# Performance work log

Measured on AMD Instinct MI355X. Metric: run time of the kernel, lower is better.

Reference implementation:

```python
import math
import jax, jax.numpy as jnp
import numpy as np

INPUT_DIM = 1024
OUTPUT_DIM = 1024
DEGREE = 8
EPS = 1.0


def setup_inputs() -> dict:
    key = jax.random.key(0)
    k1, k2 = jax.random.split(key)
    x = jax.random.normal(k1, (8192, INPUT_DIM), dtype=jnp.float32)
    std = 1.0 / (INPUT_DIM * (DEGREE + 1))
    hermite_coeffs = std * jax.random.normal(k2, (INPUT_DIM, OUTPUT_DIM, DEGREE + 1), dtype=jnp.float32)
    return {"x": x, "hermite_coeffs": hermite_coeffs}


def _hermite_basis(x):
    # x: [B, I] squashed input; returns [B, I, DEGREE+1] Hermite-function basis.
    pi_q = math.pi ** (-0.25)
    gauss = jnp.exp(-0.5 * x * x)
    h0 = pi_q * gauss
    hs = [h0]
    if DEGREE > 0:
        hs.append(math.sqrt(2.0) * pi_q * x * gauss)
    for i in range(2, DEGREE + 1):
        hs.append(math.sqrt(2.0 / i) * x * hs[i - 1] - math.sqrt((i - 1) / i) * hs[i - 2])
    return jnp.stack(hs, axis=-1)


def reference(x, hermite_coeffs):
    x = x.reshape(-1, INPUT_DIM)
    x = jnp.tanh(x) * (math.sqrt(2 * DEGREE + 1) + EPS)
    hermite = _hermite_basis(x)  # [B, I, D+1]
    y = jnp.einsum('bid,iod->bo', hermite, hermite_coeffs)
    return y.reshape(-1, OUTPUT_DIM)
```

## Files before the change

### kernel.cpp

```cpp
#include <hip/hip_runtime.h>

#define MDIM 8192
#define IDIM 1024
#define ODIM 1024
#define D1   9
#define KDIM (IDIM * D1)

typedef _Float16 half8   __attribute__((ext_vector_type(8)));
typedef _Float16 half2v  __attribute__((ext_vector_type(2)));
typedef float    float4v __attribute__((ext_vector_type(4)));

#define BSCALE 256.0f
#define INV_BSCALE (1.0f / 256.0f)
#define USCALE 5.123105625617661f
#define H0C 0.7511255444649425f
#define H1C 1.0622519497598084f

__device__ __forceinline__ void hermite9(float xv, float h[D1]) {
    float ax = fabsf(xv);
    float t  = __expf(-2.0f * ax);
    float th = (1.0f - t) / (1.0f + t);
    th = copysignf(th, xv);
    float u = th * USCALE;
    float g = __expf(-0.5f * u * u);
    h[0] = H0C * g;
    h[1] = H1C * u * g;
    const float c1[D1] = {0.f, 0.f, 1.0f, 0.8164965809277260f, 0.7071067811865476f,
                          0.6324555320336759f, 0.5773502691896258f, 0.5345224838248488f, 0.5f};
    const float c2[D1] = {0.f, 0.f, 0.7071067811865476f, 0.8164965809277260f, 0.8660254037844386f,
                          0.8944271909999159f, 0.9128709291752769f, 0.9258200997725514f, 0.9354143466934853f};
#pragma unroll
    for (int d = 2; d < D1; ++d) h[d] = c1[d] * u * h[d - 1] - c2[d] * h[d - 2];
}

__global__ __launch_bounds__(256) void prep_b(const float* __restrict__ C,
                                              _Float16* __restrict__ Bt) {
    __shared__ float lds[288 * 33];
    const int t  = threadIdx.x;
    const int ti = blockIdx.x & 31;
    const int to = blockIdx.x >> 5;
    const float* base = C + (size_t)ti * 32 * 9216 + (size_t)to * 32 * 9;
#pragma unroll
    for (int j = 0; j < 36; ++j) {
        int f   = t + 256 * j;
        int row = f / 288;
        int col = f - row * 288;
        lds[col * 33 + row] = base[(size_t)row * 9216 + col];
    }
    __syncthreads();
    _Float16* bb = Bt + (size_t)to * 32 * KDIM + ti * 32;
#pragma unroll
    for (int j = 0; j < 36; ++j) {
        int e   = t + 256 * j;
        int i   = e & 31;
        int odp = e >> 5;
        int ol  = odp / 9;
        int d   = odp - ol * 9;
        bb[(size_t)ol * KDIM + d * IDIM + i] = (_Float16)(lds[odp * 33 + i] * BSCALE);
    }
}

__global__ __launch_bounds__(256, 2) void gemm_fused(
    const float* __restrict__ x,
    const _Float16* __restrict__ Bt,
    float* __restrict__ out)
{
    const int tid = threadIdx.x;
    const int w = tid >> 6;
    const int l = tid & 63;
    const int bn = blockIdx.x;
    const int bm = blockIdx.y;

    __shared__ _Float16 As[128 * 64];
    __shared__ _Float16 Bs[128 * 64];

    const int lrow8 = l >> 3;
    const int kgrp  = (l & 7) ^ lrow8;
    const _Float16* Bg = Bt + ((size_t)(bn * 128 + w * 8 + lrow8) * KDIM + kgrp * 8);

    const int q   = l >> 4;
    const int m16 = l & 15;
    const int s3  = m16 & 7;
    const int wm  = w >> 1, wn = w & 1;

    const int r  = tid >> 1;
    const int ih = tid & 1;
    const int r7 = r & 7;
    _Float16* arow = As + r * 64;

    float4v acc[4][4] = {};

    constexpr float c1a[D1] = {0.f, 0.f, 1.0f, 0.8164965809277260f, 0.7071067811865476f,
                               0.6324555320336759f, 0.5773502691896258f, 0.5345224838248488f, 0.5f};
    constexpr float c2a[D1] = {0.f, 0.f, 0.7071067811865476f, 0.8164965809277260f, 0.8660254037844386f,
                               0.8944271909999159f, 0.9128709291752769f, 0.9258200997725514f, 0.9354143466934853f};

    for (int ib = 0; ib < 16; ++ib) {
        const int kbase = ib * 64;

#pragma unroll
        for (int rr = 0; rr < 4; ++rr)
            __builtin_amdgcn_global_load_lds(
                (const __attribute__((address_space(1))) void*)(Bg + (size_t)(rr * 32) * KDIM + kbase),
                (__attribute__((address_space(3))) void*)((char*)Bs + (rr * 4 + w) * 1024),
                16, 0, 0);

        const float4* xp = (const float4*)(x + (((size_t)(bm * 128 + r)) << 10) + kbase + ih * 32);
        float u[32];
#pragma unroll
        for (int j = 0; j < 8; ++j) {
            float4 v = xp[j];
            u[4*j+0] = v.x; u[4*j+1] = v.y; u[4*j+2] = v.z; u[4*j+3] = v.w;
        }
#pragma unroll
        for (int j = 0; j < 32; ++j) {
            float xv = u[j];
            float t2 = __expf(-2.0f * fabsf(xv));
            float th = (1.0f - t2) / (1.0f + t2);
            u[j] = copysignf(th, xv) * USCALE;
        }
        half2v u2[16], hA[16], hB[16];
#pragma unroll
        for (int p = 0; p < 16; ++p) {
            float u0 = u[2*p], u1 = u[2*p+1];
            float g0 = __expf(-0.5f * u0 * u0);
            float g1 = __expf(-0.5f * u1 * u1);
            u2[p] = half2v{(_Float16)u0, (_Float16)u1};
            hA[p] = half2v{(_Float16)(H0C * g0), (_Float16)(H0C * g1)};
            hB[p] = half2v{(_Float16)(H1C * u0 * g0), (_Float16)(H1C * u1 * g1)};
        }

#pragma unroll
        for (int d = 0; d < D1; ++d) {
            if (d >= 1) {
#pragma unroll
                for (int rr = 0; rr < 4; ++rr)
                    __builtin_amdgcn_global_load_lds(
                        (const __attribute__((address_space(1))) void*)(Bg + (size_t)(rr * 32) * KDIM + d * IDIM + kbase),
                        (__attribute__((address_space(3))) void*)((char*)Bs + (rr * 4 + w) * 1024),
                        16, 0, 0);
            }
            half2v ht[16];
            if (d == 0) {
#pragma unroll
                for (int p = 0; p < 16; ++p) ht[p] = hA[p];
            } else if (d == 1) {
#pragma unroll
                for (int p = 0; p < 16; ++p) ht[p] = hB[p];
            } else {
                const half2v c1v = half2v{(_Float16)c1a[d], (_Float16)c1a[d]};
                const half2v c2v = half2v{(_Float16)c2a[d], (_Float16)c2a[d]};
#pragma unroll
                for (int p = 0; p < 16; ++p) {
                    half2v t = u2[p] * hB[p];
                    ht[p] = c1v * t - c2v * hA[p];
                    hA[p] = hB[p];
                    hB[p] = ht[p];
                }
            }
#pragma unroll
            for (int c = 0; c < 4; ++c) {
                int slot = (ih * 4 + c) ^ r7;
                half8 vv;
#pragma unroll
                for (int pp = 0; pp < 4; ++pp) {
                    vv[2*pp+0] = ht[4*c+pp][0];
                    vv[2*pp+1] = ht[4*c+pp][1];
                }
                *(half8*)(arow + slot * 8) = vv;
            }
            __syncthreads();

#pragma unroll
            for (int ko = 0; ko < 2; ++ko) {
                const int slot = (q + 4 * ko) ^ s3;
                half8 af[4], bf[4];
#pragma unroll
                for (int i = 0; i < 4; ++i) {
                    af[i] = *(const half8*)&As[(wm * 64 + i * 16 + m16) * 64 + slot * 8];
                    bf[i] = *(const half8*)&Bs[(wn * 64 + i * 16 + m16) * 64 + slot * 8];
                }
#pragma unroll
                for (int i = 0; i < 4; ++i)
#pragma unroll
                    for (int j = 0; j < 4; ++j)
                        acc[i][j] = __builtin_amdgcn_mfma_f32_16x16x32_f16(af[i], bf[j], acc[i][j], 0, 0, 0);
            }
            __syncthreads();
        }
    }

#pragma unroll
    for (int i = 0; i < 4; ++i) {
        int row = bm * 128 + wm * 64 + i * 16 + q * 4;
#pragma unroll
        for (int j = 0; j < 4; ++j) {
            int col = bn * 128 + wn * 64 + j * 16 + m16;
            float* op = out + (size_t)row * ODIM + col;
#pragma unroll
            for (int r2 = 0; r2 < 4; ++r2)
                op[(size_t)r2 * ODIM] = acc[i][j][r2] * INV_BSCALE;
        }
    }
}

__global__ void naive_kernel(const float* __restrict__ x, const float* __restrict__ C,
                             float* __restrict__ out) {
    __shared__ float hb[IDIM * D1];
    int b = blockIdx.x;
    int tid = threadIdx.x;
    for (int i = tid; i < IDIM; i += 256) {
        float h[D1];
        hermite9(x[(size_t)b * IDIM + i], h);
#pragma unroll
        for (int d = 0; d < D1; ++d) hb[i * D1 + d] = h[d];
    }
    __syncthreads();
    for (int o = tid; o < ODIM; o += 256) {
        float acc = 0.f;
        for (int i = 0; i < IDIM; ++i) {
            const float* cp = C + ((size_t)i * ODIM + o) * D1;
            const float* hp = hb + i * D1;
#pragma unroll
            for (int d = 0; d < D1; ++d) acc += hp[d] * cp[d];
        }
        out[(size_t)b * ODIM + o] = acc;
    }
}

extern "C" void kernel_launch(void* const* d_in, const int* in_sizes, int n_in,
                              void* d_out, int out_size, void* d_ws, size_t ws_size,
                              hipStream_t stream) {
    const float* x      = (const float*)d_in[0];
    const float* coeffs = (const float*)d_in[1];
    float* out = (float*)d_out;

    const size_t bt_bytes = (size_t)ODIM * KDIM * sizeof(_Float16);

    if (ws_size >= bt_bytes) {
        _Float16* Bt = (_Float16*)d_ws;
        hipLaunchKernelGGL(prep_b, dim3(1024), dim3(256), 0, stream, coeffs, Bt);
        hipLaunchKernelGGL(gemm_fused, dim3(8, 64), dim3(256), 0, stream, x, Bt, out);
    } else {
        hipLaunchKernelGGL(naive_kernel, dim3(MDIM), dim3(256), 0, stream, x, coeffs, out);
    }
}
```

Baseline: 313.9 us.

## Precompute tanh/gauss basis in separate kernel and double-buffer LDS tiles

Adds a prep_u kernel that computes the squashed input and the Gaussian term once per element in fp16. Each of the 8 column blocks then reads these instead of recomputing tanh and exp from the fp32 input. The GEMM kernel double-buffers the A and B LDS tiles, prefetching the next B tile and generating the next Hermite degree while the current tile runs through MFMA, which halves the barriers per step. In exchange it adds a kernel launch, extra workspace and global traffic for U and H0, doubles LDS use (which may limit occupancy), and rounds h1 to fp16 sooner.

```diff
diff --git a/kernel.cpp b/kernel.cpp
--- a/kernel.cpp
+++ b/kernel.cpp
@@ -14,7 +14,7 @@
 #define INV_BSCALE (1.0f / 256.0f)
 #define USCALE 5.123105625617661f
 #define H0C 0.7511255444649425f
-#define H1C 1.0622519497598084f
+#define SQRT2 1.4142135623730951f
 
 __device__ __forceinline__ void hermite9(float xv, float h[D1]) {
     float ax = fabsf(xv);
@@ -24,7 +24,7 @@
     float u = th * USCALE;
     float g = __expf(-0.5f * u * u);
     h[0] = H0C * g;
-    h[1] = H1C * u * g;
+    h[1] = SQRT2 * H0C * u * g;
     const float c1[D1] = {0.f, 0.f, 1.0f, 0.8164965809277260f, 0.7071067811865476f,
                           0.6324555320336759f, 0.5773502691896258f, 0.5345224838248488f, 0.5f};
     const float c2[D1] = {0.f, 0.f, 0.7071067811865476f, 0.8164965809277260f, 0.8660254037844386f,
@@ -60,8 +60,31 @@
     }
 }
 
-__global__ __launch_bounds__(256, 2) void gemm_fused(
-    const float* __restrict__ x,
+__global__ __launch_bounds__(256) void prep_u(const float* __restrict__ x,
+                                              _Float16* __restrict__ U,
+                                              _Float16* __restrict__ H0) {
+    size_t t = (size_t)blockIdx.x * 256 + threadIdx.x;
+    const float4* xp = (const float4*)(x + t * 8);
+    float4 a0 = xp[0], a1 = xp[1];
+    float xv[8] = {a0.x, a0.y, a0.z, a0.w, a1.x, a1.y, a1.z, a1.w};
+    half8 uu, hh;
+#pragma unroll
+    for (int e = 0; e < 8; ++e) {
+        float v  = xv[e];
+        float t2 = __expf(-2.0f * fabsf(v));
+        float th = (1.0f - t2) / (1.0f + t2);
+        float u  = copysignf(th, v) * USCALE;
+        float g  = __expf(-0.5f * u * u);
+        uu[e] = (_Float16)u;
+        hh[e] = (_Float16)(H0C * g);
+    }
+    *(half8*)(U  + t * 8) = uu;
+    *(half8*)(H0 + t * 8) = hh;
+}
+
+__global__ __launch_bounds__(256, 2) void gemm_fused2(
+    const _Float16* __restrict__ U,
+    const _Float16* __restrict__ H0,
     const _Float16* __restrict__ Bt,
     float* __restrict__ out)
 {
@@ -71,8 +94,8 @@
     const int bn = blockIdx.x;
     const int bm = blockIdx.y;
 
-    __shared__ _Float16 As[128 * 64];
-    __shared__ _Float16 Bs[128 * 64];
+    __shared__ _Float16 As[2][128 * 64];
+    __shared__ _Float16 Bs[2][128 * 64];
 
     const int lrow8 = l >> 3;
     const int kgrp  = (l & 7) ^ lrow8;
@@ -86,90 +109,102 @@
     const int r  = tid >> 1;
     const int ih = tid & 1;
     const int r7 = r & 7;
-    _Float16* arow = As + r * 64;
-
-    float4v acc[4][4] = {};
+    const size_t urow = (((size_t)(bm * 128 + r)) << 10) + ih * 32;
 
     constexpr float c1a[D1] = {0.f, 0.f, 1.0f, 0.8164965809277260f, 0.7071067811865476f,
                                0.6324555320336759f, 0.5773502691896258f, 0.5345224838248488f, 0.5f};
     constexpr float c2a[D1] = {0.f, 0.f, 0.7071067811865476f, 0.8164965809277260f, 0.8660254037844386f,
                                0.8944271909999159f, 0.9128709291752769f, 0.9258200997725514f, 0.9354143466934853f};
 
+    half2v u2[16], hA[16], hB[16];
+    const half2v sq2 = half2v{(_Float16)SQRT2, (_Float16)SQRT2};
+
+    auto loadUH = [&](int kb) {
+        const half8* up = (const half8*)(U  + urow + kb);
+        const half8* hp = (const half8*)(H0 + urow + kb);
+        half8 ub[4], hb[4];
+#pragma unroll
+        for (int a = 0; a < 4; ++a) { ub[a] = up[a]; hb[a] = hp[a]; }
+#pragma unroll
+        for (int a = 0; a < 4; ++a)
+#pragma unroll
+            for (int b = 0; b < 4; ++b) {
+                u2[4*a+b] = half2v{ub[a][2*b], ub[a][2*b+1]};
+                hA[4*a+b] = half2v{hb[a][2*b], hb[a][2*b+1]};
+            }
+#pragma unroll
+        for (int p = 0; p < 16; ++p) hB[p] = sq2 * u2[p] * hA[p];
+    };
+
+    _Float16* arow0 = &As[0][r * 64];
+    _Float16* arow1 = &As[1][r * 64];
+    auto writeA = [&](int buf, const half2v ht[16]) {
+        _Float16* arow = buf ? arow1 : arow0;
+#pragma unroll
+        for (int c = 0; c < 4; ++c) {
+            int slot = (ih * 4 + c) ^ r7;
+            half8 vv;
+#pragma unroll
+            for (int pp = 0; pp < 4; ++pp) {
+                vv[2*pp+0] = ht[4*c+pp][0];
+                vv[2*pp+1] = ht[4*c+pp][1];
+            }
+            *(half8*)(arow + slot * 8) = vv;
+        }
+    };
+
+    float4v acc[4][4] = {};
+
+#pragma unroll
+    for (int rr = 0; rr < 4; ++rr)
+        __builtin_amdgcn_global_load_lds(
+            (const __attribute__((address_space(1))) void*)(Bg + (size_t)(rr * 32) * KDIM),
+            (__attribute__((address_space(3))) void*)((char*)&Bs[0][0] + (rr * 4 + w) * 1024),
+            16, 0, 0);
+    loadUH(0);
+    writeA(0, hA);
+    __syncthreads();
+
     for (int ib = 0; ib < 16; ++ib) {
         const int kbase = ib * 64;
-
-#pragma unroll
-        for (int rr = 0; rr < 4; ++rr)
-            __builtin_amdgcn_global_load_lds(
-                (const __attribute__((address_space(1))) void*)(Bg + (size_t)(rr * 32) * KDIM + kbase),
-                (__attribute__((address_space(3))) void*)((char*)Bs + (rr * 4 + w) * 1024),
-                16, 0, 0);
-
-        const float4* xp = (const float4*)(x + (((size_t)(bm * 128 + r)) << 10) + kbase + ih * 32);
-        float u[32];
-#pragma unroll
-        for (int j = 0; j < 8; ++j) {
-            float4 v = xp[j];
-            u[4*j+0] = v.x; u[4*j+1] = v.y; u[4*j+2] = v.z; u[4*j+3] = v.w;
-        }
-#pragma unroll
-        for (int j = 0; j < 32; ++j) {
-            float xv = u[j];
-            float t2 = __expf(-2.0f * fabsf(xv));
-            float th = (1.0f - t2) / (1.0f + t2);
-            u[j] = copysignf(th, xv) * USCALE;
-        }
-        half2v u2[16], hA[16], hB[16];
-#pragma unroll
-        for (int p = 0; p < 16; ++p) {
-            float u0 = u[2*p], u1 = u[2*p+1];
-            float g0 = __expf(-0.5f * u0 * u0);
-            float g1 = __expf(-0.5f * u1 * u1);
-            u2[p] = half2v{(_Float16)u0, (_Float16)u1};
-            hA[p] = half2v{(_Float16)(H0C * g0), (_Float16)(H0C * g1)};
-            hB[p] = half2v{(_Float16)(H1C * u0 * g0), (_Float16)(H1C * u1 * g1)};
-        }
-
 #pragma unroll
         for (int d = 0; d < D1; ++d) {
-            if (d >= 1) {
+            const int cur = (ib + d) & 1;
+            const int nxt = cur ^ 1;
+            const bool has_next = (d < 8) || (ib < 15);
+
+            if (has_next) {
+                const int nkoff = (d == 8) ? (kbase + 64)
+                                           : ((d + 1) * IDIM + kbase);
 #pragma unroll
                 for (int rr = 0; rr < 4; ++rr)
                     __builtin_amdgcn_global_load_lds(
-                        (const __attribute__((address_space(1))) void*)(Bg + (size_t)(rr * 32) * KDIM + d * IDIM + kbase),
-                        (__attribute__((address_space(3))) void*)((char*)Bs + (rr * 4 + w) * 1024),
+                        (const __attribute__((address_space(1))) void*)(Bg + (size_t)(rr * 32) * KDIM + nkoff),
+                        (__attribute__((address_space(3))) void*)((char*)&Bs[nxt][0] + (rr * 4 + w) * 1024),
                         16, 0, 0);
             }
+
             half2v ht[16];
-            if (d == 0) {
-#pragma unroll
-                for (int p = 0; p < 16; ++p) ht[p] = hA[p];
-            } else if (d == 1) {
-#pragma unroll
-                for (int p = 0; p < 16; ++p) ht[p] = hB[p];
-            } else {
-                const half2v c1v = half2v{(_Float16)c1a[d], (_Float16)c1a[d]};
-                const half2v c2v = half2v{(_Float16)c2a[d], (_Float16)c2a[d]};
-#pragma unroll
-                for (int p = 0; p < 16; ++p) {
-                    half2v t = u2[p] * hB[p];
-                    ht[p] = c1v * t - c2v * hA[p];
-                    hA[p] = hB[p];
-                    hB[p] = ht[p];
+            if (has_next) {
+                if (d == 8) {
+                    loadUH(kbase + 64);
+#pragma unroll
+                    for (int p = 0; p < 16; ++p) ht[p] = hA[p];
+                } else if (d == 0) {
+#pragma unroll
+                    for (int p = 0; p < 16; ++p) ht[p] = hB[p];
+                } else {
+                    const half2v c1v = half2v{(_Float16)c1a[d+1], (_Float16)c1a[d+1]};
+                    const half2v c2v = half2v{(_Float16)c2a[d+1], (_Float16)c2a[d+1]};
+#pragma unroll
+                    for (int p = 0; p < 16; ++p) {
+                        half2v t = u2[p] * hB[p];
+                        ht[p] = c1v * t - c2v * hA[p];
+                        hA[p] = hB[p];
+                        hB[p] = ht[p];
+                    }
                 }
             }
-#pragma unroll
-            for (int c = 0; c < 4; ++c) {
-                int slot = (ih * 4 + c) ^ r7;
-                half8 vv;
-#pragma unroll
-                for (int pp = 0; pp < 4; ++pp) {
-                    vv[2*pp+0] = ht[4*c+pp][0];
-                    vv[2*pp+1] = ht[4*c+pp][1];
-                }
-                *(half8*)(arow + slot * 8) = vv;
-            }
-            __syncthreads();
 
 #pragma unroll
             for (int ko = 0; ko < 2; ++ko) {
@@ -177,8 +212,8 @@
                 half8 af[4], bf[4];
 #pragma unroll
                 for (int i = 0; i < 4; ++i) {
-                    af[i] = *(const half8*)&As[(wm * 64 + i * 16 + m16) * 64 + slot * 8];
-                    bf[i] = *(const half8*)&Bs[(wn * 64 + i * 16 + m16) * 64 + slot * 8];
+                    af[i] = *(const half8*)&As[cur][(wm * 64 + i * 16 + m16) * 64 + slot * 8];
+                    bf[i] = *(const half8*)&Bs[cur][(wn * 64 + i * 16 + m16) * 64 + slot * 8];
                 }
 #pragma unroll
                 for (int i = 0; i < 4; ++i)
@@ -186,6 +221,9 @@
                     for (int j = 0; j < 4; ++j)
                         acc[i][j] = __builtin_amdgcn_mfma_f32_16x16x32_f16(af[i], bf[j], acc[i][j], 0, 0, 0);
             }
+
+            if (has_next) writeA(nxt, ht);
+
             __syncthreads();
         }
     }
@@ -236,11 +274,15 @@
     float* out = (float*)d_out;
 
     const size_t bt_bytes = (size_t)ODIM * KDIM * sizeof(_Float16);
-
-    if (ws_size >= bt_bytes) {
+    const size_t u_bytes  = (size_t)MDIM * IDIM * sizeof(_Float16);
+
+    if (ws_size >= bt_bytes + 2 * u_bytes) {
         _Float16* Bt = (_Float16*)d_ws;
+        _Float16* Uv = (_Float16*)((char*)d_ws + bt_bytes);
+        _Float16* H0 = (_Float16*)((char*)d_ws + bt_bytes + u_bytes);
         hipLaunchKernelGGL(prep_b, dim3(1024), dim3(256), 0, stream, coeffs, Bt);
-        hipLaunchKernelGGL(gemm_fused, dim3(8, 64), dim3(256), 0, stream, x, Bt, out);
+        hipLaunchKernelGGL(prep_u, dim3((MDIM * IDIM) / 2048), dim3(256), 0, stream, x, Uv, H0);
+        hipLaunchKernelGGL(gemm_fused2, dim3(8, 64), dim3(256), 0, stream, Uv, H0, Bt, out);
     } else {
         hipLaunchKernelGGL(naive_kernel, dim3(MDIM), dim3(256), 0, stream, x, coeffs, out);
     }
```

New measurement: 281.1 us. 1.12x faster.
